# Performance work log

Measured on AMD Instinct MI355X. Metric: run time of the kernel, lower is better.

The kernel has to match this reference:

```python
import jax, jax.numpy as jnp
import numpy as np

N = 50000        # nodes
E = 800000       # edges
D_IN = 128       # input feature dim
HID = 64         # hidden_dim
HEADS = 4
OUT = 2          # output_dim (fraud / not-fraud)
BN_EPS = 1e-5
NEG_SLOPE = 0.2  # PyG GATv2Conv default


def setup_inputs() -> dict:
    key = jax.random.key(0)
    ks = jax.random.split(key, 16)
    g = lambda k, shape, s=0.05: (jax.random.normal(k, shape, jnp.float32) * s)
    HC = HEADS * HID  # 256
    return {
        "x": jax.random.normal(ks[0], (N, D_IN), jnp.float32),
        "edge_index": jax.random.randint(ks[1], (2, E), 0, N),
        # input projection
        "W_in": g(ks[2], (D_IN, HID)), "b_in": jnp.zeros((HID,), jnp.float32),
        # GATv2 layer 0: HID -> HID, 4 heads (concat -> 256)
        "Wl0": g(ks[3], (HID, HC)), "Wr0": g(ks[4], (HID, HC)),
        "att0": g(ks[5], (HEADS, HID)), "bias0": jnp.zeros((HC,), jnp.float32),
        # GATv2 layer 1: 256 -> HID, 4 heads (concat -> 256)
        "Wl1": g(ks[6], (HC, HC)), "Wr1": g(ks[7], (HC, HC)),
        "att1": g(ks[8], (HEADS, HID)), "bias1": jnp.zeros((HC,), jnp.float32),
        # GATv2 layer 2: 256 -> OUT, 1 head
        "Wl2": g(ks[9], (HC, OUT)), "Wr2": g(ks[10], (HC, OUT)),
        "att2": g(ks[11], (1, OUT)), "bias2": jnp.zeros((OUT,), jnp.float32),
        # BatchNorm (eval mode: running stats) for the first num_layers-1 = 2 layers
        "bn_gamma": jnp.ones((2, HC), jnp.float32),
        "bn_beta": jnp.zeros((2, HC), jnp.float32),
        "bn_mean": jnp.zeros((2, HC), jnp.float32),
        "bn_var": jnp.ones((2, HC), jnp.float32),
    }


def _gatv2(h, src, dst, Wl, Wr, att, bias):
    """PyG GATv2Conv (concat=True, negative_slope=0.2). src->dst messages."""
    n = h.shape[0]
    heads, c = att.shape
    xl = (h @ Wl).reshape(n, heads, c)   # source transform
    xr = (h @ Wr).reshape(n, heads, c)   # target transform
    e = jax.nn.leaky_relu(xl[src] + xr[dst], NEG_SLOPE)       # [E, H, C]
    logits = jnp.einsum('ehc,hc->eh', e, att)                 # [E, H]
    # segment softmax over incoming edges of each destination node
    m = jax.ops.segment_max(logits, dst, num_segments=n)      # [N, H]
    ex = jnp.exp(logits - m[dst])
    denom = jax.ops.segment_sum(ex, dst, num_segments=n)
    alpha = ex / denom[dst]                                   # [E, H]
    out = jax.ops.segment_sum(xl[src] * alpha[..., None], dst, num_segments=n)
    return out.reshape(n, heads * c) + bias


def _bn_eval(h, gamma, beta, mean, var):
    return gamma * (h - mean) * jax.lax.rsqrt(var + BN_EPS) + beta


def reference(x, edge_index, W_in, b_in, Wl0, Wr0, att0, bias0,
              Wl1, Wr1, att1, bias1, Wl2, Wr2, att2, bias2,
              bn_gamma, bn_beta, bn_mean, bn_var):
    n = x.shape[0]
    loop = jnp.arange(n)
    src = jnp.concatenate([edge_index[0], loop])  # PyG add_self_loops=True
    dst = jnp.concatenate([edge_index[1], loop])

    h = jax.nn.relu(x @ W_in + b_in)              # dropout is identity in eval

    # layer 0 (no residual: 64 != 256)
    h = _gatv2(h, src, dst, Wl0, Wr0, att0, bias0)
    h = jax.nn.relu(_bn_eval(h, bn_gamma[0], bn_beta[0], bn_mean[0], bn_var[0]))

    # layer 1 (residual: 256 == 256)
    h_prev = h
    h = _gatv2(h, src, dst, Wl1, Wr1, att1, bias1)
    h = jax.nn.relu(_bn_eval(h, bn_gamma[1], bn_beta[1], bn_mean[1], bn_var[1]))
    h = h + h_prev

    # output layer, 1 head
    h = _gatv2(h, src, dst, Wl2, Wr2, att2, bias2)
    return jax.nn.log_softmax(h, axis=1)
```

## Files before the change

kernel.cpp:

```cpp
#include <hip/hip_runtime.h>
#include <hip/hip_bf16.h>
#include <math.h>


using h16     = _Float16;
using half2v  = __attribute__((ext_vector_type(2))) h16;
using half4v  = __attribute__((ext_vector_type(4))) h16;
using half8   = __attribute__((ext_vector_type(8))) h16;
using floatx2 = __attribute__((ext_vector_type(2))) float;
using floatx4 = __attribute__((ext_vector_type(4))) float;

__device__ __forceinline__ float lrelu(float x) { return x > 0.f ? x : 0.2f * x; }

__device__ __forceinline__ half2v shfl_xor_h2(half2v v, int mask) {
    float f = __builtin_bit_cast(float, v);
    f = __shfl_xor(f, mask, 64);
    return __builtin_bit_cast(half2v, f);
}

__global__ __launch_bounds__(256) void scan_blk(const int* __restrict__ deg,
                                                int* __restrict__ rowstart,
                                                int* __restrict__ bsum, int N) {
    int t = blockIdx.x * 256 + threadIdx.x;
    int lane = threadIdx.x & 63, wid = threadIdx.x >> 6;
    int v = (t < N) ? ((deg[t] + 4) & ~3) : 0;
    int x = v;
#pragma unroll
    for (int off = 1; off < 64; off <<= 1) {
        int y = __shfl_up(x, off, 64);
        if (lane >= off) x += y;
    }
    __shared__ int wsum[4];
    if (lane == 63) wsum[wid] = x;
    __syncthreads();
    int add = 0;
#pragma unroll
    for (int w = 0; w < 4; ++w) if (w < wid) add += wsum[w];
    int incl = x + add;
    if (t < N) rowstart[t] = incl - v;
    if (threadIdx.x == 255) bsum[blockIdx.x] = incl;
}

__global__ __launch_bounds__(256) void scan_off(int* __restrict__ bsum, int NB) {
    int t = threadIdx.x;
    int lane = t & 63, wid = t >> 6;
    int v = (t < NB) ? bsum[t] : 0;
    int x = v;
#pragma unroll
    for (int off = 1; off < 64; off <<= 1) {
        int y = __shfl_up(x, off, 64);
        if (lane >= off) x += y;
    }
    __shared__ int wsum[4];
    if (lane == 63) wsum[wid] = x;
    __syncthreads();
    int add = 0;
#pragma unroll
    for (int w = 0; w < 4; ++w) if (w < wid) add += wsum[w];
    if (t < NB) bsum[t] = x + add - v;
}

__global__ void add_off(const int* __restrict__ bsum, const int* __restrict__ deg,
                        int* __restrict__ rowstart, int* __restrict__ cursor,
                        int* __restrict__ csr_src, int N) {
    int t = blockIdx.x * 256 + threadIdx.x;
    if (t >= N) return;
    int r = rowstart[t] + bsum[blockIdx.x];
    rowstart[t] = r;
    cursor[t] = r;
    int dg = deg[t];
    int npad = (dg + 4) & ~3;
    for (int k = dg; k < npad; ++k) csr_src[r + k] = t;
}

__device__ __forceinline__ void pack_one(const float* __restrict__ W,
                                         h16* __restrict__ Wp,
                                         int t, int K, int NC) {
    int j = t & 7;
    int l = (t >> 3) & 63;
    int rest = t >> 9;
    int NT = NC >> 4;
    int nt = rest % NT;
    int kc = rest / NT;
    int row = kc * 32 + (l >> 4) * 8 + j;
    int col = nt * 16 + (l & 15);
    Wp[t] = (h16)W[(size_t)row * NC + col];
}

__global__ void pack_all(const float* __restrict__ W_in,
                         const float* __restrict__ Wl0, const float* __restrict__ Wr0,
                         const float* __restrict__ Wl1, const float* __restrict__ Wr1,
                         h16* __restrict__ P_in,
                         h16* __restrict__ P_l0, h16* __restrict__ P_r0,
                         h16* __restrict__ P_l1, h16* __restrict__ P_r1,
                         const float4* __restrict__ x, half4v* __restrict__ xh, int n4,
                         const int* __restrict__ ei, int E, int* __restrict__ deg) {
    int t = blockIdx.x * blockDim.x + threadIdx.x;
    if (t < 8192)        pack_one(W_in, P_in, t, 128, 64);
    else if (t < 24576)  pack_one(Wl0, P_l0, t - 8192, 64, 256);
    else if (t < 40960)  pack_one(Wr0, P_r0, t - 24576, 64, 256);
    else if (t < 106496) pack_one(Wl1, P_l1, t - 40960, 256, 256);
    else if (t < 172032) pack_one(Wr1, P_r1, t - 106496, 256, 256);
    else if (t < 172032 + n4) {
        int u = t - 172032;
        float4 v = x[u];
        half4v o = { (h16)v.x, (h16)v.y, (h16)v.z, (h16)v.w };
        xh[u] = o;
    } else {
        int u = t - 172032 - n4;
        if (u < E) atomicAdd(&deg[ei[E + u]], 1);
    }
}

template<int KC, int NT, bool RELU>
__device__ __forceinline__ void gemm_body(const h16* __restrict__ Xh,
                                          const h16* __restrict__ Wp,
                                          const float* __restrict__ bias,
                                          h16* __restrict__ outp, int M, int bx) {
    constexpr int K = KC * 32;
    constexpr int ldo = NT * 16;
    constexpr int CHUNK8 = NT * 64;
    constexpr int PER_THR = CHUNK8 / 256;
    __shared__ half8 wbuf[2][CHUNK8];

    const half8* WG = (const half8*)Wp;
    const int tid = threadIdx.x;
    const int wid = tid >> 6, lane = tid & 63;
    const int quad = lane >> 4, li = lane & 15;
    const int r0 = bx * 64 + wid * 16;
    int arow = r0 + li; if (arow >= M) arow = M - 1;
    const half8* A8 = (const half8*)Xh + (size_t)arow * (K / 8) + quad;

    floatx4 acc[NT];
#pragma unroll
    for (int t = 0; t < NT; ++t) acc[t] = (floatx4){0.f, 0.f, 0.f, 0.f};

    half8 st[PER_THR];
#pragma unroll
    for (int i = 0; i < PER_THR; ++i) st[i] = WG[i * 256 + tid];
#pragma unroll
    for (int i = 0; i < PER_THR; ++i) wbuf[0][i * 256 + tid] = st[i];
    __syncthreads();

#pragma unroll
    for (int kc = 0; kc < KC; ++kc) {
        int cur = kc & 1;
        if (kc + 1 < KC) {
#pragma unroll
            for (int i = 0; i < PER_THR; ++i)
                st[i] = WG[(size_t)(kc + 1) * CHUNK8 + i * 256 + tid];
        }
        half8 a = A8[kc * 4];
#pragma unroll
        for (int nt = 0; nt < NT; ++nt) {
            half8 b = wbuf[cur][nt * 64 + lane];
            acc[nt] = __builtin_amdgcn_mfma_f32_16x16x32_f16(a, b, acc[nt], 0, 0, 0);
        }
        if (kc + 1 < KC) {
#pragma unroll
            for (int i = 0; i < PER_THR; ++i) wbuf[cur ^ 1][i * 256 + tid] = st[i];
        }
        __syncthreads();
    }

#pragma unroll
    for (int nt = 0; nt < NT; ++nt) {
#pragma unroll
        for (int reg = 0; reg < 4; ++reg) {
            int rr = r0 + quad * 4 + reg;
            if (rr >= M) continue;
            float v = acc[nt][reg];
            if (RELU) v = fmaxf(v + bias[nt * 16 + li], 0.f);
            outp[(size_t)rr * ldo + nt * 16 + li] = (h16)v;
        }
    }
}

template<int KC, int NT, bool RELU, bool DUAL>
__global__ __launch_bounds__(256) void gemm_lds(
        const h16* __restrict__ Xh,
        const h16* __restrict__ Wp0, const h16* __restrict__ Wp1,
        const float* __restrict__ bias,
        h16* __restrict__ out0, h16* __restrict__ out1, int M) {
    const h16* Wp = (DUAL && blockIdx.y) ? Wp1 : Wp0;
    h16* outp = (DUAL && blockIdx.y) ? out1 : out0;
    gemm_body<KC, NT, RELU>(Xh, Wp, bias, outp, M, blockIdx.x);
}

__global__ __launch_bounds__(256) void scatter_gemm0(
        const int* __restrict__ ei, int E,
        int* __restrict__ cursor, int* __restrict__ csr_src, int GS,
        const h16* __restrict__ xh, const h16* __restrict__ Wp_in,
        const float* __restrict__ b_in, h16* __restrict__ H0h, int M) {
    if ((int)blockIdx.x < GS) {
        int base = blockIdx.x * 2048 + threadIdx.x;
        int e[8], d[8], p[8], s[8];
#pragma unroll
        for (int k = 0; k < 8; ++k) e[k] = base + k * 256;
#pragma unroll
        for (int k = 0; k < 8; ++k) d[k] = (e[k] < E) ? ei[E + e[k]] : 0;
#pragma unroll
        for (int k = 0; k < 8; ++k) p[k] = (e[k] < E) ? atomicAdd(&cursor[d[k]], 1) : 0;
#pragma unroll
        for (int k = 0; k < 8; ++k) s[k] = (e[k] < E) ? ei[e[k]] : 0;
#pragma unroll
        for (int k = 0; k < 8; ++k) if (e[k] < E) csr_src[p[k]] = s[k];
    } else {
        gemm_body<4, 4, true>(xh, Wp_in, b_in, H0h, M, blockIdx.x - GS);
    }
}

__global__ __launch_bounds__(128) void attn4_bn(
                         int N, const h16* __restrict__ XL,
                         const h16* __restrict__ XR,
                         const float* __restrict__ att,
                         const int* __restrict__ rowstart, const int* __restrict__ deg,
                         const int* __restrict__ csr_src,
                         const float* __restrict__ gamma, const float* __restrict__ beta,
                         const float* __restrict__ mean, const float* __restrict__ var,
                         const float* __restrict__ bias, const h16* __restrict__ resid,
                         h16* __restrict__ outb) {
    int wv = blockIdx.x * (blockDim.x >> 6) + (threadIdx.x >> 6);
    int d0 = wv * 2;
    if (d0 >= N) return;
    int lane = threadIdx.x & 63;
    int sl   = lane & 31;
    int dh   = d0 + (lane >> 5);
    bool dvalid = dh < N;
    int dr = dvalid ? dh : d0;

    int start = rowstart[dr];
    int dg    = deg[dr];
    int nreal = dg + 1;
    int npad  = (dg + 4) & ~3;
    int npmax = max(npad, __shfl_xor(npad, 32, 64));

    union H8 { uint4 u; half2v h[4]; };
    H8 bv, wt;
    bv.u = *(const uint4*)(XR + (size_t)dr * 256 + sl * 8);
    {
        const float LOG2E = 1.44269504088896340736f;
        const float* ar = att + (sl >> 3) * 64 + (sl & 7) * 8;
        float4 wa = *(const float4*)ar;
        float4 wb = *(const float4*)(ar + 4);
        wt.h[0] = half2v{(h16)(wa.x * LOG2E), (h16)(wa.y * LOG2E)};
        wt.h[1] = half2v{(h16)(wa.z * LOG2E), (h16)(wa.w * LOG2E)};
        wt.h[2] = half2v{(h16)(wb.x * LOG2E), (h16)(wb.y * LOG2E)};
        wt.h[3] = half2v{(h16)(wb.z * LOG2E), (h16)(wb.w * LOG2E)};
    }
    const h16 k02 = (h16)0.2f;
    const uint4* XLv = (const uint4*)XL;

    auto ep = [&](const H8& x) -> h16 {
        half2v q{(h16)0, (h16)0};
#pragma unroll
        for (int j = 0; j < 4; ++j) {
            half2v e  = x.h[j] + bv.h[j];
            half2v lr = __builtin_elementwise_max(e, e * k02);
            q += lr * wt.h[j];
        }
        return q.x + q.y;
    };

    float l = 0.f;
    half2v acc[4] = {half2v{(h16)0,(h16)0}, half2v{(h16)0,(h16)0},
                     half2v{(h16)0,(h16)0}, half2v{(h16)0,(h16)0}};

    int4 iv = *(const int4*)(csr_src + start);
    for (int i = 0; i < npmax; i += 4) {
        int4 cur = iv;
        if (i + 4 < npmax) {
            int nxt = min(i + 4, npad - 4);
            iv = *(const int4*)(csr_src + start + nxt);
        }
        H8 x0, x1, x2, x3;
        x0.u = XLv[(size_t)(unsigned)cur.x * 32 + sl];
        x1.u = XLv[(size_t)(unsigned)cur.y * 32 + sl];
        x2.u = XLv[(size_t)(unsigned)cur.z * 32 + sl];
        x3.u = XLv[(size_t)(unsigned)cur.w * 32 + sl];
        half2v p01 = { ep(x0), ep(x1) };
        half2v p23 = { ep(x2), ep(x3) };
#pragma unroll
        for (int s = 1; s < 8; s <<= 1) {
            p01 += shfl_xor_h2(p01, s);
            p23 += shfl_xor_h2(p23, s);
        }
        int rem = nreal - i;
        float e0 = (rem > 0) ? exp2f((float)p01.x) : 0.f;
        float e1 = (rem > 1) ? exp2f((float)p01.y) : 0.f;
        float e2 = (rem > 2) ? exp2f((float)p23.x) : 0.f;
        float e3 = (rem > 3) ? exp2f((float)p23.y) : 0.f;
        l += (e0 + e1) + (e2 + e3);
        h16 h0 = (h16)e0, h1 = (h16)e1, h2 = (h16)e2, h3 = (h16)e3;
        half2v eb0{h0,h0}, eb1{h1,h1}, eb2{h2,h2}, eb3{h3,h3};
#pragma unroll
        for (int j = 0; j < 4; ++j) {
            acc[j] += eb0 * x0.h[j];
            acc[j] += eb1 * x1.h[j];
            acc[j] += eb2 * x2.h[j];
            acc[j] += eb3 * x3.h[j];
        }
    }

    float inv = 1.f / l;
    float oc[8];
#pragma unroll
    for (int j = 0; j < 4; ++j) { oc[2*j] = (float)acc[j].x; oc[2*j+1] = (float)acc[j].y; }
    const float4* g4  = (const float4*)gamma;
    const float4* be4 = (const float4*)beta;
    const float4* mu4 = (const float4*)mean;
    const float4* va4 = (const float4*)var;
    const float4* bi4 = (const float4*)bias;
    float o[8];
#pragma unroll
    for (int q = 0; q < 2; ++q) {
        float4 g  = g4[sl*2+q],  bb = be4[sl*2+q], mu = mu4[sl*2+q];
        float4 va = va4[sl*2+q], bi = bi4[sl*2+q];
        float s0 = g.x * rsqrtf(va.x + 1e-5f);
        float s1 = g.y * rsqrtf(va.y + 1e-5f);
        float s2 = g.z * rsqrtf(va.z + 1e-5f);
        float s3 = g.w * rsqrtf(va.w + 1e-5f);
        o[q*4+0] = fmaxf(oc[q*4+0]*inv*s0 + (bi.x-mu.x)*s0 + bb.x, 0.f);
        o[q*4+1] = fmaxf(oc[q*4+1]*inv*s1 + (bi.y-mu.y)*s1 + bb.y, 0.f);
        o[q*4+2] = fmaxf(oc[q*4+2]*inv*s2 + (bi.z-mu.z)*s2 + bb.z, 0.f);
        o[q*4+3] = fmaxf(oc[q*4+3]*inv*s3 + (bi.w-mu.w)*s3 + bb.w, 0.f);
    }
    if (resid) {
        H8 rv; rv.u = *(const uint4*)(resid + (size_t)dr * 256 + sl * 8);
#pragma unroll
        for (int j = 0; j < 4; ++j) {
            o[2*j]   += (float)rv.h[j].x;
            o[2*j+1] += (float)rv.h[j].y;
        }
    }
    if (dvalid) {
        H8 ov;
#pragma unroll
        for (int j = 0; j < 4; ++j) ov.h[j] = half2v{(h16)o[2*j], (h16)o[2*j+1]};
        *(uint4*)(outb + (size_t)dh * 256 + sl * 8) = ov.u;
    }
}

__global__ void gemm2_wave(const h16* __restrict__ X, const float* __restrict__ Wl,
                           const float* __restrict__ Wr, float* __restrict__ xl2,
                           float* __restrict__ xr2, int N) {
    int t = blockIdx.x * blockDim.x + threadIdx.x;
    int n = t >> 4;
    int sl = t & 15;
    if (n >= N) return;
    const half4v* Xr = (const half4v*)(X + (size_t)n * 256);
    const float4* Wl4 = (const float4*)Wl;
    const float4* Wr4 = (const float4*)Wr;
    float l0 = 0.f, l1 = 0.f, r0 = 0.f, r1 = 0.f;
#pragma unroll
    for (int j = 0; j < 4; ++j) {
        int idx = sl + j * 16;
        half4v xh = Xr[idx];
        float4 xv = { (float)xh.x, (float)xh.y, (float)xh.z, (float)xh.w };
        float4 wa = Wl4[idx * 2];
        float4 wb = Wl4[idx * 2 + 1];
        l0 += xv.x * wa.x + xv.y * wa.z + xv.z * wb.x + xv.w * wb.z;
        l1 += xv.x * wa.y + xv.y * wa.w + xv.z * wb.y + xv.w * wb.w;
        wa = Wr4[idx * 2]; wb = Wr4[idx * 2 + 1];
        r0 += xv.x * wa.x + xv.y * wa.z + xv.z * wb.x + xv.w * wb.z;
        r1 += xv.x * wa.y + xv.y * wa.w + xv.z * wb.y + xv.w * wb.w;
    }
#pragma unroll
    for (int off = 1; off < 16; off <<= 1) {
        l0 += __shfl_xor(l0, off, 64);
        l1 += __shfl_xor(l1, off, 64);
        r0 += __shfl_xor(r0, off, 64);
        r1 += __shfl_xor(r1, off, 64);
    }
    if (sl == 0) {
        xl2[n * 2] = l0; xl2[n * 2 + 1] = l1;
        xr2[n * 2] = r0; xr2[n * 2 + 1] = r1;
    }
}

__global__ void attn1_16(int N, const float* __restrict__ xl2, const float* __restrict__ xr2,
                         const float* __restrict__ att, const float* __restrict__ bias,
                         const int* __restrict__ rowstart, const int* __restrict__ deg,
                         const int* __restrict__ csr_src, float* __restrict__ out) {
    int t = blockIdx.x * blockDim.x + threadIdx.x;
    int d = t >> 4, sl = t & 15;
    if (d >= N) return;
    float a0 = att[0], a1 = att[1];
    float2 xr = ((const float2*)xr2)[d];
    float b0 = xr.x, b1 = xr.y;
    int st = rowstart[d];
    int nreal = deg[d] + 1;
    int npad  = (deg[d] + 4) & ~3;
    float l = 0.f, ac0 = 0.f, ac1 = 0.f;
    for (int i = sl; i < npad; i += 16) {
        int s = csr_src[st + i];
        float2 xv = ((const float2*)xl2)[s];
        float q = lrelu(xv.x + b0) * a0 + lrelu(xv.y + b1) * a1;
        float e = (i < nreal) ? __expf(q) : 0.f;
        l += e; ac0 += e * xv.x; ac1 += e * xv.y;
    }
#pragma unroll
    for (int off = 1; off < 16; off <<= 1) {
        l   += __shfl_xor(l, off, 64);
        ac0 += __shfl_xor(ac0, off, 64);
        ac1 += __shfl_xor(ac1, off, 64);
    }
    if (sl == 0) {
        float inv = 1.f / l;
        float v0 = ac0 * inv + bias[0];
        float v1 = ac1 * inv + bias[1];
        float mx = fmaxf(v0, v1);
        float lse = mx + logf(__expf(v0 - mx) + __expf(v1 - mx));
        out[d * 2] = v0 - lse;
        out[d * 2 + 1] = v1 - lse;
    }
}

extern "C" void kernel_launch(void* const* d_in, const int* in_sizes, int n_in,
                              void* d_out, int out_size, void* d_ws, size_t ws_size,
                              hipStream_t stream) {
    const float* x        = (const float*)d_in[0];
    const int*   ei       = (const int*)  d_in[1];
    const float* W_in     = (const float*)d_in[2];
    const float* b_in     = (const float*)d_in[3];
    const float* Wl0      = (const float*)d_in[4];
    const float* Wr0      = (const float*)d_in[5];
    const float* att0     = (const float*)d_in[6];
    const float* bias0    = (const float*)d_in[7];
    const float* Wl1      = (const float*)d_in[8];
    const float* Wr1      = (const float*)d_in[9];
    const float* att1     = (const float*)d_in[10];
    const float* bias1    = (const float*)d_in[11];
    const float* Wl2      = (const float*)d_in[12];
    const float* Wr2      = (const float*)d_in[13];
    const float* att2     = (const float*)d_in[14];
    const float* bias2    = (const float*)d_in[15];
    const float* bn_gamma = (const float*)d_in[16];
    const float* bn_beta  = (const float*)d_in[17];
    const float* bn_mean  = (const float*)d_in[18];
    const float* bn_var   = (const float*)d_in[19];

    const int N  = in_sizes[0] / 128;
    const int E  = in_sizes[1] / 2;
    const int NB = (N + 255) / 256;

    float* ws = (float*)d_ws;
    size_t off = 0;
    float* XL2  = ws + off; off += (size_t)N * 2;
    float* XR2  = ws + off; off += (size_t)N * 2;
    h16* Ah   = (h16*)(ws + off); off += (size_t)N * 128;
    h16* Bh   = (h16*)(ws + off); off += (size_t)N * 128;
    h16* Ch   = (h16*)(ws + off); off += (size_t)N * 128;
    h16* Dh   = (h16*)(ws + off); off += (size_t)N * 128;
    h16* H0h  = (h16*)(ws + off); off += (size_t)N * 32;
    h16* xh   = (h16*)(ws + off); off += (size_t)N * 64;
    h16* Wp_in = (h16*)(ws + off); off += 4096;
    h16* Wp_l0 = (h16*)(ws + off); off += 8192;
    h16* Wp_r0 = (h16*)(ws + off); off += 8192;
    h16* Wp_l1 = (h16*)(ws + off); off += 32768;
    h16* Wp_r1 = (h16*)(ws + off); off += 32768;
    int* ip = (int*)(ws + off);
    int* deg      = ip;              ip += N;
    int* rowstart = ip;              ip += N;
    int* cursor   = ip;              ip += N;
    int* bsum     = ip;              ip += NB;
    int* csr_src  = ip;              ip += E + 4 * N + 64;

    (void)hipMemsetAsync(deg, 0, (size_t)N * sizeof(int), stream);

    const int PACK_T = 172032 + N * 32 + E;
    pack_all<<<(PACK_T + 255) / 256, 256, 0, stream>>>(
        W_in, Wl0, Wr0, Wl1, Wr1, Wp_in, Wp_l0, Wp_r0, Wp_l1, Wp_r1,
        (const float4*)x, (half4v*)xh, N * 32, ei, E, deg);

    scan_blk<<<NB, 256, 0, stream>>>(deg, rowstart, bsum, N);
    scan_off<<<1, 256, 0, stream>>>(bsum, NB);
    add_off<<<NB, 256, 0, stream>>>(bsum, deg, rowstart, cursor, csr_src, N);

    const int GBM = (N + 63) / 64;
    const int GS  = (E + 2047) / 2048;

    scatter_gemm0<<<GS + GBM, 256, 0, stream>>>(ei, E, cursor, csr_src, GS,
                                                xh, Wp_in, b_in, H0h, N);

    gemm_lds<2, 16, false, true><<<dim3(GBM, 2), 256, 0, stream>>>(
        H0h, Wp_l0, Wp_r0, nullptr, Ah, Bh, N);
    attn4_bn<<<(N + 3) / 4, 128, 0, stream>>>(N, Ah, Bh, att0,
                                              rowstart, deg, csr_src,
                                              bn_gamma, bn_beta, bn_mean, bn_var,
                                              bias0, nullptr, Ch);

    gemm_lds<8, 16, false, true><<<dim3(GBM, 2), 256, 0, stream>>>(
        Ch, Wp_l1, Wp_r1, nullptr, Ah, Bh, N);
    attn4_bn<<<(N + 3) / 4, 128, 0, stream>>>(N, Ah, Bh, att1,
                                              rowstart, deg, csr_src,
                                              bn_gamma + 256, bn_beta + 256, bn_mean + 256,
                                              bn_var + 256, bias1, Ch, Dh);

    gemm2_wave<<<(N * 16 + 255) / 256, 256, 0, stream>>>(Dh, Wl2, Wr2, XL2, XR2, N);
    attn1_16<<<(N * 16 + 255) / 256, 256, 0, stream>>>(N, XL2, XR2, att2, bias2,
                                                       rowstart, deg, csr_src, (float*)d_out);
}
```

Measured before the change: 402.8 us.

## Store source-side projections in FP8 to halve gather traffic in attention

The GEMM that produces the source-node projection XL now writes FP8 (e4m3) bytes instead of fp16. The attention kernels gather those 8-byte rows per lane and convert them back to fp16 in registers. This halves the bytes moved by the random per-edge neighbor gathers, which dominate the attention layers. Attention blocks also grow from 128 to 256 threads. The cost is extra conversion instructions and lower precision in both the attention logits and the aggregated messages, which risks tolerance failures.

```diff
diff --git a/kernel.cpp b/kernel.cpp
--- a/kernel.cpp
+++ b/kernel.cpp
@@ -16,6 +16,24 @@
     float f = __builtin_bit_cast(float, v);
     f = __shfl_xor(f, mask, 64);
     return __builtin_bit_cast(half2v, f);
+}
+
+union H8 { uint4 u; half2v h[4]; };
+
+__device__ __forceinline__ half4v cvt_fp8x4(unsigned v) {
+    floatx2 lo = __builtin_amdgcn_cvt_pk_f32_fp8((int)v, false);
+    floatx2 hi = __builtin_amdgcn_cvt_pk_f32_fp8((int)v, true);
+    half4v r = { (h16)lo.x, (h16)lo.y, (h16)hi.x, (h16)hi.y };
+    return r;
+}
+
+__device__ __forceinline__ H8 cvt_fp8x8(uint2 v) {
+    half4v a = cvt_fp8x4(v.x);
+    half4v b = cvt_fp8x4(v.y);
+    H8 r;
+    r.h[0] = a.xy; r.h[1] = a.zw;
+    r.h[2] = b.xy; r.h[3] = b.zw;
+    return r;
 }
 
 __global__ __launch_bounds__(256) void scan_blk(const int* __restrict__ deg,
@@ -112,11 +130,11 @@
     }
 }
 
-template<int KC, int NT, bool RELU>
+template<int KC, int NT, bool RELU, bool OUT8>
 __device__ __forceinline__ void gemm_body(const h16* __restrict__ Xh,
                                           const h16* __restrict__ Wp,
                                           const float* __restrict__ bias,
-                                          h16* __restrict__ outp, int M, int bx) {
+                                          void* __restrict__ outp, int M, int bx) {
     constexpr int K = KC * 32;
     constexpr int ldo = NT * 16;
     constexpr int CHUNK8 = NT * 64;
@@ -171,20 +189,27 @@
             if (rr >= M) continue;
             float v = acc[nt][reg];
             if (RELU) v = fmaxf(v + bias[nt * 16 + li], 0.f);
-            outp[(size_t)rr * ldo + nt * 16 + li] = (h16)v;
-        }
-    }
-}
-
-template<int KC, int NT, bool RELU, bool DUAL>
+            if (OUT8) {
+                int pk = __builtin_amdgcn_cvt_pk_fp8_f32(v, v, 0, false);
+                ((unsigned char*)outp)[(size_t)rr * ldo + nt * 16 + li] = (unsigned char)pk;
+            } else {
+                ((h16*)outp)[(size_t)rr * ldo + nt * 16 + li] = (h16)v;
+            }
+        }
+    }
+}
+
+template<int KC, int NT, bool RELU, bool DUAL, bool OUT8L>
 __global__ __launch_bounds__(256) void gemm_lds(
         const h16* __restrict__ Xh,
         const h16* __restrict__ Wp0, const h16* __restrict__ Wp1,
         const float* __restrict__ bias,
-        h16* __restrict__ out0, h16* __restrict__ out1, int M) {
-    const h16* Wp = (DUAL && blockIdx.y) ? Wp1 : Wp0;
-    h16* outp = (DUAL && blockIdx.y) ? out1 : out0;
-    gemm_body<KC, NT, RELU>(Xh, Wp, bias, outp, M, blockIdx.x);
+        void* __restrict__ out0, void* __restrict__ out1, int M) {
+    if (DUAL && blockIdx.y) {
+        gemm_body<KC, NT, RELU, false>(Xh, Wp1, bias, out1, M, blockIdx.x);
+    } else {
+        gemm_body<KC, NT, RELU, OUT8L>(Xh, Wp0, bias, out0, M, blockIdx.x);
+    }
 }
 
 __global__ __launch_bounds__(256) void scatter_gemm0(
@@ -206,12 +231,12 @@
 #pragma unroll
         for (int k = 0; k < 8; ++k) if (e[k] < E) csr_src[p[k]] = s[k];
     } else {
-        gemm_body<4, 4, true>(xh, Wp_in, b_in, H0h, M, blockIdx.x - GS);
-    }
-}
-
-__global__ __launch_bounds__(128) void attn4_bn(
-                         int N, const h16* __restrict__ XL,
+        gemm_body<4, 4, true, false>(xh, Wp_in, b_in, H0h, M, blockIdx.x - GS);
+    }
+}
+
+__global__ __launch_bounds__(256) void attn4_bn(
+                         int N, const unsigned char* __restrict__ XL8,
                          const h16* __restrict__ XR,
                          const float* __restrict__ att,
                          const int* __restrict__ rowstart, const int* __restrict__ deg,
@@ -235,7 +260,6 @@
     int npad  = (dg + 4) & ~3;
     int npmax = max(npad, __shfl_xor(npad, 32, 64));
 
-    union H8 { uint4 u; half2v h[4]; };
     H8 bv, wt;
     bv.u = *(const uint4*)(XR + (size_t)dr * 256 + sl * 8);
     {
@@ -249,7 +273,7 @@
         wt.h[3] = half2v{(h16)(wb.z * LOG2E), (h16)(wb.w * LOG2E)};
     }
     const h16 k02 = (h16)0.2f;
-    const uint4* XLv = (const uint4*)XL;
+    const uint2* XLv = (const uint2*)XL8;
 
     auto ep = [&](const H8& x) -> h16 {
         half2v q{(h16)0, (h16)0};
@@ -273,11 +297,14 @@
             int nxt = min(i + 4, npad - 4);
             iv = *(const int4*)(csr_src + start + nxt);
         }
-        H8 x0, x1, x2, x3;
-        x0.u = XLv[(size_t)(unsigned)cur.x * 32 + sl];
-        x1.u = XLv[(size_t)(unsigned)cur.y * 32 + sl];
-        x2.u = XLv[(size_t)(unsigned)cur.z * 32 + sl];
-        x3.u = XLv[(size_t)(unsigned)cur.w * 32 + sl];
+        uint2 v0 = XLv[(size_t)(unsigned)cur.x * 32 + sl];
+        uint2 v1 = XLv[(size_t)(unsigned)cur.y * 32 + sl];
+        uint2 v2 = XLv[(size_t)(unsigned)cur.z * 32 + sl];
+        uint2 v3 = XLv[(size_t)(unsigned)cur.w * 32 + sl];
+        H8 x0 = cvt_fp8x8(v0);
+        H8 x1 = cvt_fp8x8(v1);
+        H8 x2 = cvt_fp8x8(v2);
+        H8 x3 = cvt_fp8x8(v3);
         half2v p01 = { ep(x0), ep(x1) };
         half2v p23 = { ep(x2), ep(x3) };
 #pragma unroll
@@ -448,7 +475,7 @@
     size_t off = 0;
     float* XL2  = ws + off; off += (size_t)N * 2;
     float* XR2  = ws + off; off += (size_t)N * 2;
-    h16* Ah   = (h16*)(ws + off); off += (size_t)N * 128;
+    unsigned char* A8 = (unsigned char*)(ws + off); off += (size_t)N * 64;
     h16* Bh   = (h16*)(ws + off); off += (size_t)N * 128;
     h16* Ch   = (h16*)(ws + off); off += (size_t)N * 128;
     h16* Dh   = (h16*)(ws + off); off += (size_t)N * 128;
@@ -483,16 +510,16 @@
     scatter_gemm0<<<GS + GBM, 256, 0, stream>>>(ei, E, cursor, csr_src, GS,
                                                 xh, Wp_in, b_in, H0h, N);
 
-    gemm_lds<2, 16, false, true><<<dim3(GBM, 2), 256, 0, stream>>>(
-        H0h, Wp_l0, Wp_r0, nullptr, Ah, Bh, N);
-    attn4_bn<<<(N + 3) / 4, 128, 0, stream>>>(N, Ah, Bh, att0,
+    gemm_lds<2, 16, false, true, true><<<dim3(GBM, 2), 256, 0, stream>>>(
+        H0h, Wp_l0, Wp_r0, nullptr, A8, Bh, N);
+    attn4_bn<<<(N + 7) / 8, 256, 0, stream>>>(N, A8, Bh, att0,
                                               rowstart, deg, csr_src,
                                               bn_gamma, bn_beta, bn_mean, bn_var,
                                               bias0, nullptr, Ch);
 
-    gemm_lds<8, 16, false, true><<<dim3(GBM, 2), 256, 0, stream>>>(
-        Ch, Wp_l1, Wp_r1, nullptr, Ah, Bh, N);
-    attn4_bn<<<(N + 3) / 4, 128, 0, stream>>>(N, Ah, Bh, att1,
+    gemm_lds<8, 16, false, true, true><<<dim3(GBM, 2), 256, 0, stream>>>(
+        Ch, Wp_l1, Wp_r1, nullptr, A8, Bh, N);
+    attn4_bn<<<(N + 7) / 8, 256, 0, stream>>>(N, A8, Bh, att1,
                                               rowstart, deg, csr_src,
                                               bn_gamma + 256, bn_beta + 256, bn_mean + 256,
                                               bn_var + 256, bias1, Ch, Dh);
```

Result: faster. 383.4 us (-4.8%).
